# Optimization experiments

Measured on AMD Instinct MI355X. Metric: run time of the kernel, lower is better.

Reference implementation:

```python
import jax, jax.numpy as jnp
import numpy as np

B, N, C = 4, 2048, 1024
H = 16
HD = C // H  # head_dim = 64


def setup_inputs() -> dict:
    key = jax.random.key(0)
    k1, k2, k3 = jax.random.split(key, 3)
    x = jax.random.normal(k1, (B, N, C), dtype=jnp.float32)
    # nn.Linear-style init scale ~ 1/sqrt(fan_in)
    W_qkv = jax.random.normal(k2, (3 * C, C), dtype=jnp.float32) / np.sqrt(C)
    W_proj = jax.random.normal(k3, (C, C), dtype=jnp.float32) / np.sqrt(C)
    b_proj = jnp.zeros((C,), dtype=jnp.float32)
    return {"x": x, "W_qkv": W_qkv, "W_proj": W_proj, "b_proj": b_proj}


def reference(x, W_qkv, W_proj, b_proj):
    Bb, Nn, Cc = x.shape
    scale = (Cc // H) ** -0.5
    # qkv: [B,N,3C] -> [3,B,H,N,HD]
    qkv = jnp.einsum('bnc,dc->bnd', x, W_qkv)
    qkv = qkv.reshape(Bb, Nn, 3, H, Cc // H).transpose(2, 0, 3, 1, 4)
    q, k, v = qkv[0] * scale, qkv[1], qkv[2]
    attn = jnp.einsum('bhqd,bhkd->bhqk', q, k)  # [B,H,N,N]
    attn = jax.nn.softmax(attn, axis=-1)
    out = jnp.einsum('bhqk,bhkd->bhqd', attn, v)  # [B,H,N,HD]
    out = out.transpose(0, 2, 1, 3).reshape(Bb, Nn, Cc)
    return jnp.einsum('bnc,dc->bnd', out, W_proj) + b_proj
```

## Files before the change

kernel.cpp:

```cpp
#include <hip/hip_runtime.h>

typedef _Float16 f16;
typedef _Float16 half8 __attribute__((ext_vector_type(8)));
typedef _Float16 half4 __attribute__((ext_vector_type(4)));
typedef float float4_ __attribute__((ext_vector_type(4)));

#define MFMA16(a, b, c) __builtin_amdgcn_mfma_f32_16x16x32_f16(a, b, c, 0, 0, 0)

__device__ __forceinline__ void gld_lds16(const void* g, void* l) {
    __builtin_amdgcn_global_load_lds(
        (const __attribute__((address_space(1))) void*)g,
        (__attribute__((address_space(3))) void*)l, 16, 0, 0);
}

__global__ void cast_kernel(const float* __restrict__ in, f16* __restrict__ out,
                            int n, int qboundary, float qscale) {
    int i = (blockIdx.x * blockDim.x + threadIdx.x) * 4;
    if (i >= n) return;
    float4_ v = *(const float4_*)(in + i);
    float sc = (i < qboundary) ? qscale : 1.0f;
    half4 h;
    h[0] = (f16)(v[0] * sc);
    h[1] = (f16)(v[1] * sc);
    h[2] = (f16)(v[2] * sc);
    h[3] = (f16)(v[3] * sc);
    *(half4*)(out + i) = h;
}

__global__ __launch_bounds__(256, 2)
void qkv_gemm(const f16* __restrict__ X, const f16* __restrict__ W,
              f16* __restrict__ Q, f16* __restrict__ Kq, f16* __restrict__ V) {
    const int K = 1024;
    __shared__ __align__(16) f16 sA[128 * 64];
    __shared__ __align__(16) f16 sB[128 * 64];
    int tid = threadIdx.x;
    int lane = tid & 63, wave = tid >> 6;
    int wm = wave >> 1, wn = wave & 1;
    int l15 = lane & 15, quad = lane >> 4;
    int rowBase = blockIdx.y * 128;
    int colBase = blockIdx.x * 128;

    float4_ acc[4][4] = {};

    for (int k0 = 0; k0 < K; k0 += 64) {
        for (int i = 0; i < 4; ++i) {
            int seg = wave * 4 + i;
            int e = (seg * 64 + lane) * 8;
            int r = e >> 6, c = e & 63;
            gld_lds16(X + (size_t)(rowBase + r) * K + k0 + c, sA + seg * 512);
            gld_lds16(W + (size_t)(colBase + r) * K + k0 + c, sB + seg * 512);
        }
        __syncthreads();
        for (int ks = 0; ks < 2; ++ks) {
            half8 a[4], b[4];
            for (int mt = 0; mt < 4; ++mt)
                a[mt] = *(const half8*)&sA[(wm * 64 + mt * 16 + l15) * 64 + ks * 32 + quad * 8];
            for (int nt = 0; nt < 4; ++nt)
                b[nt] = *(const half8*)&sB[(wn * 64 + nt * 16 + l15) * 64 + ks * 32 + quad * 8];
            for (int mt = 0; mt < 4; ++mt)
                for (int nt = 0; nt < 4; ++nt)
                    acc[mt][nt] = MFMA16(a[mt], b[nt], acc[mt][nt]);
        }
        __syncthreads();
    }

    for (int mt = 0; mt < 4; ++mt) {
        int m0 = rowBase + wm * 64 + mt * 16 + quad * 4;
        for (int nt = 0; nt < 4; ++nt) {
            int d = colBase + wn * 64 + nt * 16 + l15;
            int part = d >> 10;
            int h = (d >> 6) & 15;
            int hd = d & 63;
            f16* dst = (part == 0) ? Q : (part == 1) ? Kq : V;
            for (int r = 0; r < 4; ++r) {
                int m = m0 + r;
                int b = m >> 11, n = m & 2047;
                dst[(size_t)((b * 16 + h) * 2048 + n) * 64 + hd] = (f16)acc[mt][nt][r];
            }
        }
    }
}

__global__ __launch_bounds__(256, 2)
void attn_kernel(const f16* __restrict__ Q, const f16* __restrict__ Kk,
                 const f16* __restrict__ V, f16* __restrict__ O) {
    const int bh = blockIdx.y;
    const int qt = blockIdx.x;
    const f16* Qb = Q + (size_t)bh * 2048 * 64;
    const f16* Kb = Kk + (size_t)bh * 2048 * 64;
    const f16* Vb = V + (size_t)bh * 2048 * 64;
    int tid = threadIdx.x, lane = tid & 63, wave = tid >> 6;
    int l15 = lane & 15, quad = lane >> 4;

    __shared__ __align__(16) f16 Vt[2][64 * 72];
    __shared__ __align__(16) f16 Pl[4][32 * 72];

    int qrow = qt * 128 + wave * 32;
    half8 aQ[2][2];
#pragma unroll
    for (int mt = 0; mt < 2; ++mt)
#pragma unroll
        for (int kc = 0; kc < 2; ++kc)
            aQ[mt][kc] = *(const half8*)(Qb + (size_t)(qrow + mt * 16 + l15) * 64 + kc * 32 + quad * 8);

    float4_ oacc[2][4] = {};
    float4_ lacc[2] = {};
    float mrow[2][4];
#pragma unroll
    for (int mt = 0; mt < 2; ++mt)
#pragma unroll
        for (int r = 0; r < 4; ++r) mrow[mt][r] = -1e30f;

    f16* Pw = &Pl[wave][0];

    half8 vone;
#pragma unroll
    for (int j = 0; j < 8; ++j) vone[j] = (f16)1.0f;

    half8 bK[2][4], v0, v1;
    {
        const f16* vsrc = Vb + (size_t)lane * 64 + wave * 16;
        v0 = *(const half8*)(vsrc);
        v1 = *(const half8*)(vsrc + 8);
#pragma unroll
        for (int kc = 0; kc < 2; ++kc)
#pragma unroll
            for (int nt = 0; nt < 4; ++nt)
                bK[kc][nt] = *(const half8*)(Kb + (size_t)(nt * 16 + l15) * 64 + kc * 32 + quad * 8);
#pragma unroll
        for (int j = 0; j < 8; ++j) {
            Vt[0][(wave * 16 + j) * 72 + lane] = v0[j];
            Vt[0][(wave * 16 + 8 + j) * 72 + lane] = v1[j];
        }
    }

    for (int it = 0; it < 32; ++it) {
        int buf = it & 1;
        __syncthreads();
        float4_ s[2][4] = {};
#pragma unroll
        for (int kc = 0; kc < 2; ++kc)
#pragma unroll
            for (int mt = 0; mt < 2; ++mt)
#pragma unroll
                for (int nt = 0; nt < 4; ++nt)
                    s[mt][nt] = MFMA16(aQ[mt][kc], bK[kc][nt], s[mt][nt]);
        half8 bKn[2][4], v0n, v1n;
        if (it < 31) {
            int t1 = (it + 1) * 64;
            const f16* vsrc = Vb + (size_t)(t1 + lane) * 64 + wave * 16;
            v0n = *(const half8*)(vsrc);
            v1n = *(const half8*)(vsrc + 8);
#pragma unroll
            for (int kc = 0; kc < 2; ++kc)
#pragma unroll
                for (int nt = 0; nt < 4; ++nt)
                    bKn[kc][nt] = *(const half8*)(Kb + (size_t)(t1 + nt * 16 + l15) * 64 + kc * 32 + quad * 8);
        }
        float mx[2][4];
        int grow = 0;
#pragma unroll
        for (int mt = 0; mt < 2; ++mt)
#pragma unroll
            for (int r = 0; r < 4; ++r) {
                float m = fmaxf(fmaxf(s[mt][0][r], s[mt][1][r]),
                                fmaxf(s[mt][2][r], s[mt][3][r]));
                for (int off = 1; off < 16; off <<= 1)
                    m = fmaxf(m, __shfl_xor(m, off, 64));
                mx[mt][r] = m;
                grow |= (m > mrow[mt][r] + 8.f) ? 1 : 0;
            }
        if (__any(grow)) {
#pragma unroll
            for (int mt = 0; mt < 2; ++mt)
#pragma unroll
                for (int r = 0; r < 4; ++r) {
                    float mnew = fmaxf(mrow[mt][r], mx[mt][r]);
                    float alpha = exp2f(mrow[mt][r] - mnew);
                    mrow[mt][r] = mnew;
#pragma unroll
                    for (int ht = 0; ht < 4; ++ht) oacc[mt][ht][r] *= alpha;
                    lacc[mt][r] *= alpha;
                }
        }
#pragma unroll
        for (int mt = 0; mt < 2; ++mt)
#pragma unroll
            for (int nt = 0; nt < 4; ++nt)
#pragma unroll
                for (int r = 0; r < 4; ++r) {
                    float p = exp2f(s[mt][nt][r] - mrow[mt][r]);
                    Pw[(mt * 16 + quad * 4 + r) * 72 + nt * 16 + l15] = (f16)p;
                }
#pragma unroll
        for (int kc = 0; kc < 2; ++kc) {
            half8 aP[2], bV[4];
#pragma unroll
            for (int mt = 0; mt < 2; ++mt)
                aP[mt] = *(const half8*)&Pw[(mt * 16 + l15) * 72 + kc * 32 + quad * 8];
#pragma unroll
            for (int ht = 0; ht < 4; ++ht)
                bV[ht] = *(const half8*)&Vt[buf][(ht * 16 + l15) * 72 + kc * 32 + quad * 8];
#pragma unroll
            for (int mt = 0; mt < 2; ++mt) {
#pragma unroll
                for (int ht = 0; ht < 4; ++ht)
                    oacc[mt][ht] = MFMA16(aP[mt], bV[ht], oacc[mt][ht]);
                lacc[mt] = MFMA16(aP[mt], vone, lacc[mt]);
            }
        }
        if (it < 31) {
#pragma unroll
            for (int j = 0; j < 8; ++j) {
                Vt[buf ^ 1][(wave * 16 + j) * 72 + lane] = v0n[j];
                Vt[buf ^ 1][(wave * 16 + 8 + j) * 72 + lane] = v1n[j];
            }
#pragma unroll
            for (int kc = 0; kc < 2; ++kc)
#pragma unroll
                for (int nt = 0; nt < 4; ++nt)
                    bK[kc][nt] = bKn[kc][nt];
        }
    }
    int b = bh >> 4, h = bh & 15;
#pragma unroll
    for (int mt = 0; mt < 2; ++mt) {
#pragma unroll
        for (int r = 0; r < 4; ++r) {
            float inv = 1.f / lacc[mt][r];
            int n = qrow + mt * 16 + quad * 4 + r;
#pragma unroll
            for (int ht = 0; ht < 4; ++ht) {
                int c = h * 64 + ht * 16 + l15;
                O[(size_t)(b * 2048 + n) * 1024 + c] = (f16)(oacc[mt][ht][r] * inv);
            }
        }
    }
}

__global__ __launch_bounds__(256, 2)
void proj_gemm(const f16* __restrict__ A, const f16* __restrict__ W,
               const float* __restrict__ bias, float* __restrict__ out) {
    const int K = 1024;
    __shared__ __align__(16) f16 sA[128 * 64];
    __shared__ __align__(16) f16 sB[128 * 64];
    int tid = threadIdx.x;
    int lane = tid & 63, wave = tid >> 6;
    int wm = wave >> 1, wn = wave & 1;
    int l15 = lane & 15, quad = lane >> 4;
    int rowBase = blockIdx.y * 128;
    int colBase = blockIdx.x * 128;

    float4_ acc[4][4] = {};

    for (int k0 = 0; k0 < K; k0 += 64) {
        for (int i = 0; i < 4; ++i) {
            int seg = wave * 4 + i;
            int e = (seg * 64 + lane) * 8;
            int r = e >> 6, c = e & 63;
            gld_lds16(A + (size_t)(rowBase + r) * K + k0 + c, sA + seg * 512);
            gld_lds16(W + (size_t)(colBase + r) * K + k0 + c, sB + seg * 512);
        }
        __syncthreads();
        for (int ks = 0; ks < 2; ++ks) {
            half8 a[4], b[4];
            for (int mt = 0; mt < 4; ++mt)
                a[mt] = *(const half8*)&sA[(wm * 64 + mt * 16 + l15) * 64 + ks * 32 + quad * 8];
            for (int nt = 0; nt < 4; ++nt)
                b[nt] = *(const half8*)&sB[(wn * 64 + nt * 16 + l15) * 64 + ks * 32 + quad * 8];
            for (int mt = 0; mt < 4; ++mt)
                for (int nt = 0; nt < 4; ++nt)
                    acc[mt][nt] = MFMA16(a[mt], b[nt], acc[mt][nt]);
        }
        __syncthreads();
    }

    for (int mt = 0; mt < 4; ++mt) {
        int m0 = rowBase + wm * 64 + mt * 16 + quad * 4;
        for (int nt = 0; nt < 4; ++nt) {
            int d = colBase + wn * 64 + nt * 16 + l15;
            float bv = bias[d];
            for (int r = 0; r < 4; ++r) {
                int m = m0 + r;
                out[(size_t)m * 1024 + d] = acc[mt][nt][r] + bv;
            }
        }
    }
}

extern "C" void kernel_launch(void* const* d_in, const int* in_sizes, int n_in,
                              void* d_out, int out_size, void* d_ws, size_t ws_size,
                              hipStream_t stream) {
    const float* x     = (const float*)d_in[0];
    const float* Wqkv  = (const float*)d_in[1];
    const float* Wproj = (const float*)d_in[2];
    const float* bproj = (const float*)d_in[3];
    float* out = (float*)d_out;

    f16* ws     = (f16*)d_ws;
    f16* xb     = ws;
    f16* wqkvb  = xb + 8388608;
    f16* wprojb = wqkvb + 3145728;
    f16* q      = wprojb + 1048576;
    f16* k      = q + 8388608;
    f16* v      = k + 8388608;
    f16* ao     = v + 8388608;

    const float qscale = 0.125f * 1.4426950408889634f;

    cast_kernel<<<8192, 256, 0, stream>>>(x, xb, 8388608, 0, 1.f);
    cast_kernel<<<3072, 256, 0, stream>>>(Wqkv, wqkvb, 3145728, 1048576, qscale);
    cast_kernel<<<1024, 256, 0, stream>>>(Wproj, wprojb, 1048576, 0, 1.f);

    qkv_gemm<<<dim3(24, 64), 256, 0, stream>>>(xb, wqkvb, q, k, v);
    attn_kernel<<<dim3(16, 64), 256, 0, stream>>>(q, k, v, ao);
    proj_gemm<<<dim3(8, 64), 256, 0, stream>>>(ao, wprojb, bproj, out);
}
```

Before: 377.5 us.

## Use 32x32 MFMA with transposed S so P stays in registers

Rewrites the attention inner loop to use 32x32x16 MFMA and computes S^T (K as the A operand), so each lane holds one query row's scores. The row max is then an in-register reduction plus one cross-half shuffle. P is packed to fp16 and rearranged with permlane32_swap straight into the A-operand layout, which removes the per-wave LDS round trip for P. The intent is to cut shuffle and LDS traffic in the softmax. In exchange the rescale step needs per-register shuffles, P now uses round-toward-zero conversion, and register pressure rises.

```diff
diff --git a/kernel.cpp b/kernel.cpp
--- a/kernel.cpp
+++ b/kernel.cpp
@@ -3,14 +3,24 @@
 typedef _Float16 f16;
 typedef _Float16 half8 __attribute__((ext_vector_type(8)));
 typedef _Float16 half4 __attribute__((ext_vector_type(4)));
+typedef __fp16 fp16x2 __attribute__((ext_vector_type(2)));
 typedef float float4_ __attribute__((ext_vector_type(4)));
+typedef float f32x16 __attribute__((ext_vector_type(16)));
+typedef unsigned int uint2_ __attribute__((ext_vector_type(2)));
 
 #define MFMA16(a, b, c) __builtin_amdgcn_mfma_f32_16x16x32_f16(a, b, c, 0, 0, 0)
+#define MFMA32(a, b, c) __builtin_amdgcn_mfma_f32_32x32x16_f16(a, b, c, 0, 0, 0)
 
 __device__ __forceinline__ void gld_lds16(const void* g, void* l) {
     __builtin_amdgcn_global_load_lds(
         (const __attribute__((address_space(1))) void*)g,
         (__attribute__((address_space(3))) void*)l, 16, 0, 0);
+}
+
+__device__ __forceinline__ unsigned pkrtz(float a, float b) {
+    union { fp16x2 h; unsigned u; } c;
+    c.h = __builtin_amdgcn_cvt_pkrtz(a, b);
+    return c.u;
 }
 
 __global__ void cast_kernel(const float* __restrict__ in, f16* __restrict__ out,
@@ -90,43 +100,34 @@
     const f16* Kb = Kk + (size_t)bh * 2048 * 64;
     const f16* Vb = V + (size_t)bh * 2048 * 64;
     int tid = threadIdx.x, lane = tid & 63, wave = tid >> 6;
-    int l15 = lane & 15, quad = lane >> 4;
+    int l31 = lane & 31, hi = lane >> 5;
 
     __shared__ __align__(16) f16 Vt[2][64 * 72];
-    __shared__ __align__(16) f16 Pl[4][32 * 72];
-
-    int qrow = qt * 128 + wave * 32;
-    half8 aQ[2][2];
-#pragma unroll
-    for (int mt = 0; mt < 2; ++mt)
-#pragma unroll
-        for (int kc = 0; kc < 2; ++kc)
-            aQ[mt][kc] = *(const half8*)(Qb + (size_t)(qrow + mt * 16 + l15) * 64 + kc * 32 + quad * 8);
-
-    float4_ oacc[2][4] = {};
-    float4_ lacc[2] = {};
-    float mrow[2][4];
-#pragma unroll
-    for (int mt = 0; mt < 2; ++mt)
-#pragma unroll
-        for (int r = 0; r < 4; ++r) mrow[mt][r] = -1e30f;
-
-    f16* Pw = &Pl[wave][0];
+
+    int qbase = qt * 128 + wave * 32;
+
+    half8 aQ[4];
+#pragma unroll
+    for (int d = 0; d < 4; ++d)
+        aQ[d] = *(const half8*)(Qb + (size_t)(qbase + l31) * 64 + d * 16 + hi * 8);
+
+    f32x16 oacc0 = {}, oacc1 = {}, lacc = {};
+    float mrow = -1e30f;
 
     half8 vone;
 #pragma unroll
     for (int j = 0; j < 8; ++j) vone[j] = (f16)1.0f;
 
-    half8 bK[2][4], v0, v1;
+    half8 bK0[4], bK1[4];
+#pragma unroll
+    for (int d = 0; d < 4; ++d) {
+        bK0[d] = *(const half8*)(Kb + (size_t)(l31) * 64 + d * 16 + hi * 8);
+        bK1[d] = *(const half8*)(Kb + (size_t)(32 + l31) * 64 + d * 16 + hi * 8);
+    }
     {
         const f16* vsrc = Vb + (size_t)lane * 64 + wave * 16;
-        v0 = *(const half8*)(vsrc);
-        v1 = *(const half8*)(vsrc + 8);
-#pragma unroll
-        for (int kc = 0; kc < 2; ++kc)
-#pragma unroll
-            for (int nt = 0; nt < 4; ++nt)
-                bK[kc][nt] = *(const half8*)(Kb + (size_t)(nt * 16 + l15) * 64 + kc * 32 + quad * 8);
+        half8 v0 = *(const half8*)(vsrc);
+        half8 v1 = *(const half8*)(vsrc + 8);
 #pragma unroll
         for (int j = 0; j < 8; ++j) {
             Vt[0][(wave * 16 + j) * 72 + lane] = v0[j];
@@ -134,81 +135,86 @@
         }
     }
 
+#pragma unroll 2
     for (int it = 0; it < 32; ++it) {
         int buf = it & 1;
         __syncthreads();
-        float4_ s[2][4] = {};
-#pragma unroll
-        for (int kc = 0; kc < 2; ++kc)
-#pragma unroll
-            for (int mt = 0; mt < 2; ++mt)
-#pragma unroll
-                for (int nt = 0; nt < 4; ++nt)
-                    s[mt][nt] = MFMA16(aQ[mt][kc], bK[kc][nt], s[mt][nt]);
-        half8 bKn[2][4], v0n, v1n;
+
+        f32x16 s0 = {}, s1 = {};
+#pragma unroll
+        for (int d = 0; d < 4; ++d) s0 = MFMA32(bK0[d], aQ[d], s0);
+#pragma unroll
+        for (int d = 0; d < 4; ++d) s1 = MFMA32(bK1[d], aQ[d], s1);
+
+        half8 bK0n[4], bK1n[4], v0n, v1n;
         if (it < 31) {
             int t1 = (it + 1) * 64;
+#pragma unroll
+            for (int d = 0; d < 4; ++d) {
+                bK0n[d] = *(const half8*)(Kb + (size_t)(t1 + l31) * 64 + d * 16 + hi * 8);
+                bK1n[d] = *(const half8*)(Kb + (size_t)(t1 + 32 + l31) * 64 + d * 16 + hi * 8);
+            }
             const f16* vsrc = Vb + (size_t)(t1 + lane) * 64 + wave * 16;
             v0n = *(const half8*)(vsrc);
             v1n = *(const half8*)(vsrc + 8);
-#pragma unroll
-            for (int kc = 0; kc < 2; ++kc)
-#pragma unroll
-                for (int nt = 0; nt < 4; ++nt)
-                    bKn[kc][nt] = *(const half8*)(Kb + (size_t)(t1 + nt * 16 + l15) * 64 + kc * 32 + quad * 8);
-        }
-        float mx[2][4];
-        int grow = 0;
-#pragma unroll
-        for (int mt = 0; mt < 2; ++mt)
-#pragma unroll
-            for (int r = 0; r < 4; ++r) {
-                float m = fmaxf(fmaxf(s[mt][0][r], s[mt][1][r]),
-                                fmaxf(s[mt][2][r], s[mt][3][r]));
-                for (int off = 1; off < 16; off <<= 1)
-                    m = fmaxf(m, __shfl_xor(m, off, 64));
-                mx[mt][r] = m;
-                grow |= (m > mrow[mt][r] + 8.f) ? 1 : 0;
-            }
-        if (__any(grow)) {
-#pragma unroll
-            for (int mt = 0; mt < 2; ++mt)
-#pragma unroll
-                for (int r = 0; r < 4; ++r) {
-                    float mnew = fmaxf(mrow[mt][r], mx[mt][r]);
-                    float alpha = exp2f(mrow[mt][r] - mnew);
-                    mrow[mt][r] = mnew;
-#pragma unroll
-                    for (int ht = 0; ht < 4; ++ht) oacc[mt][ht][r] *= alpha;
-                    lacc[mt][r] *= alpha;
-                }
-        }
-#pragma unroll
-        for (int mt = 0; mt < 2; ++mt)
-#pragma unroll
-            for (int nt = 0; nt < 4; ++nt)
-#pragma unroll
-                for (int r = 0; r < 4; ++r) {
-                    float p = exp2f(s[mt][nt][r] - mrow[mt][r]);
-                    Pw[(mt * 16 + quad * 4 + r) * 72 + nt * 16 + l15] = (f16)p;
-                }
-#pragma unroll
-        for (int kc = 0; kc < 2; ++kc) {
-            half8 aP[2], bV[4];
-#pragma unroll
-            for (int mt = 0; mt < 2; ++mt)
-                aP[mt] = *(const half8*)&Pw[(mt * 16 + l15) * 72 + kc * 32 + quad * 8];
-#pragma unroll
-            for (int ht = 0; ht < 4; ++ht)
-                bV[ht] = *(const half8*)&Vt[buf][(ht * 16 + l15) * 72 + kc * 32 + quad * 8];
-#pragma unroll
-            for (int mt = 0; mt < 2; ++mt) {
-#pragma unroll
-                for (int ht = 0; ht < 4; ++ht)
-                    oacc[mt][ht] = MFMA16(aP[mt], bV[ht], oacc[mt][ht]);
-                lacc[mt] = MFMA16(aP[mt], vone, lacc[mt]);
-            }
-        }
+        }
+
+        float mx = s0[0];
+#pragma unroll
+        for (int r = 1; r < 16; ++r) mx = fmaxf(mx, s0[r]);
+#pragma unroll
+        for (int r = 0; r < 16; ++r) mx = fmaxf(mx, s1[r]);
+        mx = fmaxf(mx, __shfl_xor(mx, 32, 64));
+
+        if (__any(mx > mrow + 8.0f)) {
+            float mnew = fmaxf(mrow, mx);
+            float alpha = exp2f(mrow - mnew);
+            mrow = mnew;
+#pragma unroll
+            for (int r = 0; r < 16; ++r) {
+                int cr = (r & 3) + 8 * (r >> 2) + 4 * hi;
+                float ar = __shfl(alpha, cr, 64);
+                oacc0[r] *= ar;
+                oacc1[r] *= ar;
+                lacc[r] *= ar;
+            }
+        }
+
+#pragma unroll
+        for (int r = 0; r < 16; ++r) s0[r] = exp2f(s0[r] - mrow);
+#pragma unroll
+        for (int r = 0; r < 16; ++r) s1[r] = exp2f(s1[r] - mrow);
+
+        half8 PA[4];
+        {
+            union { half8 h; unsigned u[4]; } w;
+            uint2_ r02 = __builtin_amdgcn_permlane32_swap(pkrtz(s0[0], s0[1]), pkrtz(s0[4], s0[5]), false, false);
+            uint2_ r13 = __builtin_amdgcn_permlane32_swap(pkrtz(s0[2], s0[3]), pkrtz(s0[6], s0[7]), false, false);
+            w.u[0] = r02[0]; w.u[1] = r13[0]; w.u[2] = r02[1]; w.u[3] = r13[1];
+            PA[0] = w.h;
+            r02 = __builtin_amdgcn_permlane32_swap(pkrtz(s0[8], s0[9]), pkrtz(s0[12], s0[13]), false, false);
+            r13 = __builtin_amdgcn_permlane32_swap(pkrtz(s0[10], s0[11]), pkrtz(s0[14], s0[15]), false, false);
+            w.u[0] = r02[0]; w.u[1] = r13[0]; w.u[2] = r02[1]; w.u[3] = r13[1];
+            PA[1] = w.h;
+            r02 = __builtin_amdgcn_permlane32_swap(pkrtz(s1[0], s1[1]), pkrtz(s1[4], s1[5]), false, false);
+            r13 = __builtin_amdgcn_permlane32_swap(pkrtz(s1[2], s1[3]), pkrtz(s1[6], s1[7]), false, false);
+            w.u[0] = r02[0]; w.u[1] = r13[0]; w.u[2] = r02[1]; w.u[3] = r13[1];
+            PA[2] = w.h;
+            r02 = __builtin_amdgcn_permlane32_swap(pkrtz(s1[8], s1[9]), pkrtz(s1[12], s1[13]), false, false);
+            r13 = __builtin_amdgcn_permlane32_swap(pkrtz(s1[10], s1[11]), pkrtz(s1[14], s1[15]), false, false);
+            w.u[0] = r02[0]; w.u[1] = r13[0]; w.u[2] = r02[1]; w.u[3] = r13[1];
+            PA[3] = w.h;
+        }
+
+#pragma unroll
+        for (int ks = 0; ks < 4; ++ks) {
+            half8 vf0 = *(const half8*)&Vt[buf][(l31) * 72 + ks * 16 + hi * 8];
+            half8 vf1 = *(const half8*)&Vt[buf][(32 + l31) * 72 + ks * 16 + hi * 8];
+            oacc0 = MFMA32(PA[ks], vf0, oacc0);
+            oacc1 = MFMA32(PA[ks], vf1, oacc1);
+            lacc = MFMA32(PA[ks], vone, lacc);
+        }
+
         if (it < 31) {
 #pragma unroll
             for (int j = 0; j < 8; ++j) {
@@ -216,25 +222,21 @@
                 Vt[buf ^ 1][(wave * 16 + 8 + j) * 72 + lane] = v1n[j];
             }
 #pragma unroll
-            for (int kc = 0; kc < 2; ++kc)
-#pragma unroll
-                for (int nt = 0; nt < 4; ++nt)
-                    bK[kc][nt] = bKn[kc][nt];
-        }
-    }
+            for (int d = 0; d < 4; ++d) {
+                bK0[d] = bK0n[d];
+                bK1[d] = bK1n[d];
+            }
+        }
+    }
+
     int b = bh >> 4, h = bh & 15;
 #pragma unroll
-    for (int mt = 0; mt < 2; ++mt) {
-#pragma unroll
-        for (int r = 0; r < 4; ++r) {
-            float inv = 1.f / lacc[mt][r];
-            int n = qrow + mt * 16 + quad * 4 + r;
-#pragma unroll
-            for (int ht = 0; ht < 4; ++ht) {
-                int c = h * 64 + ht * 16 + l15;
-                O[(size_t)(b * 2048 + n) * 1024 + c] = (f16)(oacc[mt][ht][r] * inv);
-            }
-        }
+    for (int r = 0; r < 16; ++r) {
+        int cr = (r & 3) + 8 * (r >> 2) + 4 * hi;
+        int n = qbase + cr;
+        float inv = 1.0f / lacc[r];
+        O[(size_t)(b * 2048 + n) * 1024 + h * 64 + l31] = (f16)(oacc0[r] * inv);
+        O[(size_t)(b * 2048 + n) * 1024 + h * 64 + 32 + l31] = (f16)(oacc1[r] * inv);
     }
 }
 
```

Measured after the change: 343.3 us. 1.1x faster.
